# Optimization experiments

Hardware: AMD Instinct MI355X
Metric: run time of the kernel (lower is better)

The kernel has to match this reference:

```python
import jax, jax.numpy as jnp
import numpy as np

N, IN, HID, H, OUT = 5000, 64, 32, 4, 64
NEG_SLOPE = 0.2  # LeakyReLU slope used by GAT
MASK_VAL = -1e9


def setup_inputs() -> dict:
    key = jax.random.key(0)
    ks = jax.random.split(key, 8)
    adj = (jax.random.uniform(ks[0], (N, N)) < 0.02).astype(jnp.float32)
    adj = jnp.maximum(adj, jnp.eye(N, dtype=jnp.float32))
    h = jax.random.normal(ks[1], (N, IN), dtype=jnp.float32)
    # layer 1 params: W1 [IN, H*HID], attention vectors a1_* [H, HID]
    W1 = jax.random.normal(ks[2], (IN, H * HID), dtype=jnp.float32) / np.sqrt(IN)
    a1_src = jax.random.normal(ks[3], (H, HID), dtype=jnp.float32) / np.sqrt(HID)
    a1_dst = jax.random.normal(ks[4], (H, HID), dtype=jnp.float32) / np.sqrt(HID)
    # layer 2 params: single head, W2 [H*HID, OUT]
    W2 = jax.random.normal(ks[5], (H * HID, OUT), dtype=jnp.float32) / np.sqrt(H * HID)
    a2_src = jax.random.normal(ks[6], (1, OUT), dtype=jnp.float32) / np.sqrt(OUT)
    a2_dst = jax.random.normal(ks[7], (1, OUT), dtype=jnp.float32) / np.sqrt(OUT)
    return {"adj": adj, "h": h, "W1": W1, "a1_src": a1_src, "a1_dst": a1_dst,
            "W2": W2, "a2_src": a2_src, "a2_dst": a2_dst}


def gat_conv(adj, x, W, a_src, a_dst, heads, out_dim):
    n = x.shape[0]
    Wh = (x @ W).reshape(n, heads, out_dim)              # [N, H, F']
    s_src = jnp.einsum('nhf,hf->nh', Wh, a_src)          # score contribution of node as center i
    s_dst = jnp.einsum('nhf,hf->nh', Wh, a_dst)          # contribution of node as neighbor j
    e = s_src[:, None, :] + s_dst[None, :, :]            # [N, N, H]
    e = jax.nn.leaky_relu(e, NEG_SLOPE)
    e = jnp.where(adj[:, :, None] > 0, e, MASK_VAL)
    alpha = jax.nn.softmax(e, axis=1)                    # softmax over neighbors j
    out = jnp.einsum('ijh,jhf->ihf', alpha, Wh)          # aggregate
    return out.reshape(n, heads * out_dim)               # concat heads


def reference(adj, h, W1, a1_src, a1_dst, W2, a2_src, a2_dst):
    x = gat_conv(adj, h, W1, a1_src, a1_dst, H, HID)     # [N, H*HID]
    x = jax.nn.elu(x)
    out = gat_conv(adj, x, W2, a2_src, a2_dst, 1, OUT)   # [N, OUT]
    return out
```

## Files before the change

### kernel.cpp

```cpp
#include <hip/hip_runtime.h>
#include <math.h>

#define NN   5000
#define INF_ 64
#define HID  32
#define NH   4
#define OUTF 64
#define NEG  0.2f
#define CAP  256

typedef float nt4 __attribute__((ext_vector_type(4)));

__device__ inline float wred_sum(float v) {
#pragma unroll
    for (int off = 32; off > 0; off >>= 1) v += __shfl_down(v, off, 64);
    return v;
}

__device__ inline unsigned mask4(nt4 v) {
    return (v.x > 0.f ? 1u : 0u) | (v.y > 0.f ? 2u : 0u) |
           (v.z > 0.f ? 4u : 0u) | (v.w > 0.f ? 8u : 0u);
}

__global__ __launch_bounds__(256) void k1(const float* __restrict__ adj,
        const float* __restrict__ h, const float* __restrict__ W1,
        const float* __restrict__ a1s, const float* __restrict__ a1d,
        int* __restrict__ counts, int* __restrict__ idx,
        float* __restrict__ Wh1, float* __restrict__ s1s, float* __restrict__ s1d) {
    const int i = blockIdx.x, t = threadIdx.x;
    const int lane = t & 63, wave = t >> 6;
    __shared__ int nbs[CAP];
    __shared__ int wt4[4];
    const nt4* row4 = (const nt4*)(adj + (size_t)i * NN);
    nt4 v0 = __builtin_nontemporal_load(&row4[t]);
    nt4 v1 = __builtin_nontemporal_load(&row4[t + 256]);
    nt4 v2 = __builtin_nontemporal_load(&row4[t + 512]);
    nt4 v3 = __builtin_nontemporal_load(&row4[t + 768]);
    nt4 v4 = {0.f, 0.f, 0.f, 0.f};
    if (t < NN / 4 - 1024) v4 = __builtin_nontemporal_load(&row4[t + 1024]);
    const float hreg = h[(size_t)i * INF_ + lane];
    if (t < 128) {
        float acc = 0.f;
#pragma unroll
        for (int k = 0; k < INF_; ++k) acc += __shfl(hreg, k, 64) * W1[k * (NH * HID) + t];
        Wh1[(size_t)i * (NH * HID) + t] = acc;
        const int hd = t >> 5, f = t & 31;
        float vs = acc * a1s[hd * HID + f];
        float vd = acc * a1d[hd * HID + f];
#pragma unroll
        for (int off = 16; off > 0; off >>= 1) {
            vs += __shfl_down(vs, off, 32);
            vd += __shfl_down(vd, off, 32);
        }
        if (f == 0) { s1s[i * NH + hd] = vs; s1d[i * NH + hd] = vd; }
    }
    const unsigned m20 = mask4(v0) | (mask4(v1) << 4) | (mask4(v2) << 8) |
                         (mask4(v3) << 12) | (mask4(v4) << 16);
    const int cl = __popc(m20);
    int incl = cl;
#pragma unroll
    for (int off = 1; off < 64; off <<= 1) {
        int u = __shfl_up(incl, off, 64);
        if (lane >= off) incl += u;
    }
    if (lane == 63) wt4[wave] = incl;
    __syncthreads();
    int base = 0;
#pragma unroll
    for (int w = 0; w < 4; ++w) base += (w < wave) ? wt4[w] : 0;
    int p = base + (incl - cl);
    unsigned m = m20;
    while (m) {
        const int b = __ffs(m) - 1; m &= m - 1;
        const int nid = 4 * (t + (b >> 2) * 256) + (b & 3);
        if (p < CAP) nbs[p] = nid;
        ++p;
    }
    __syncthreads();
    const int tot = wt4[0] + wt4[1] + wt4[2] + wt4[3];
    const int c = tot < CAP ? tot : CAP;
    if (t == 0) counts[i] = c;
    int4* my4 = (int4*)(idx + (size_t)i * CAP);
    for (int e = t; e < ((c + 3) >> 2); e += 256) my4[e] = ((const int4*)nbs)[e];
}

__global__ __launch_bounds__(256) void k2(const int* __restrict__ counts,
        const int* __restrict__ idx, const float* __restrict__ Wh1,
        const float* __restrict__ s1s, const float* __restrict__ s1d,
        const float* __restrict__ W2, const float* __restrict__ a2s,
        const float* __restrict__ a2d, float* __restrict__ Wh2,
        float* __restrict__ s2s, float* __restrict__ s2d) {
    const int i = blockIdx.x, t = threadIdx.x;
    const int lane = t & 63, wave = t >> 6;
    const int c = counts[i];
    const int cp = (c + 3) & ~3;
    __shared__ int   nb[CAP];
    __shared__ float sc[NH][CAP + 1];
    __shared__ float aggf[4][128];
    __shared__ float xs[128];
    __shared__ float redh[4 * NH];
    __shared__ float pw[4][64];
    const float4 ss = ((const float4*)s1s)[i];
    const float4* s1d4 = (const float4*)s1d;
    const int* my = idx + (size_t)i * CAP;
    float l0 = 0.f, l1 = 0.f, l2 = 0.f, l3 = 0.f;
    for (int e = t; e < c; e += 256) {
        const int j = my[e];
        nb[e] = j;
        const float4 sd = s1d4[j];
        float w0 = ss.x + sd.x, w1 = ss.y + sd.y, w2 = ss.z + sd.z, w3 = ss.w + sd.w;
        w0 = (w0 >= 0.f) ? w0 : NEG * w0;
        w1 = (w1 >= 0.f) ? w1 : NEG * w1;
        w2 = (w2 >= 0.f) ? w2 : NEG * w2;
        w3 = (w3 >= 0.f) ? w3 : NEG * w3;
        const float p0 = __expf(w0), p1 = __expf(w1), p2 = __expf(w2), p3 = __expf(w3);
        sc[0][e] = p0; sc[1][e] = p1; sc[2][e] = p2; sc[3][e] = p3;
        l0 += p0; l1 += p1; l2 += p2; l3 += p3;
    }
    for (int e = c + t; e < cp; e += 256) {
        nb[e] = 0;
        sc[0][e] = 0.f; sc[1][e] = 0.f; sc[2][e] = 0.f; sc[3][e] = 0.f;
    }
    l0 = wred_sum(l0); l1 = wred_sum(l1); l2 = wred_sum(l2); l3 = wred_sum(l3);
    if (lane == 0) {
        redh[wave * NH + 0] = l0; redh[wave * NH + 1] = l1;
        redh[wave * NH + 2] = l2; redh[wave * NH + 3] = l3;
    }
    __syncthreads();
    {
        const float4* Wh1v = (const float4*)Wh1;
        const int half = lane >> 5, fi = lane & 31, hd = fi >> 3;
        const int g4 = cp >> 2;
        const int gw = (g4 + 3) >> 2;
        int g = wave * gw;
        const int gend = min(g4, wave * gw + gw);
        float4 a0 = {0.f,0.f,0.f,0.f}, a1 = a0, a2 = a0, a3 = a0;
        for (; g + 1 < gend; g += 2) {
            const int e = 4 * g;
            const int j0 = nb[e + half],     j1 = nb[e + 2 + half];
            const int j2 = nb[e + 4 + half], j3 = nb[e + 6 + half];
            const float p0 = sc[hd][e + half],     p1 = sc[hd][e + 2 + half];
            const float p2 = sc[hd][e + 4 + half], p3 = sc[hd][e + 6 + half];
            const float4 w0 = Wh1v[(size_t)j0 * 32 + fi];
            const float4 w1 = Wh1v[(size_t)j1 * 32 + fi];
            const float4 w2 = Wh1v[(size_t)j2 * 32 + fi];
            const float4 w3 = Wh1v[(size_t)j3 * 32 + fi];
            a0.x += p0 * w0.x; a0.y += p0 * w0.y; a0.z += p0 * w0.z; a0.w += p0 * w0.w;
            a1.x += p1 * w1.x; a1.y += p1 * w1.y; a1.z += p1 * w1.z; a1.w += p1 * w1.w;
            a2.x += p2 * w2.x; a2.y += p2 * w2.y; a2.z += p2 * w2.z; a2.w += p2 * w2.w;
            a3.x += p3 * w3.x; a3.y += p3 * w3.y; a3.z += p3 * w3.z; a3.w += p3 * w3.w;
        }
        if (g < gend) {
            const int e = 4 * g;
            const int j0 = nb[e + half], j1 = nb[e + 2 + half];
            const float p0 = sc[hd][e + half], p1 = sc[hd][e + 2 + half];
            const float4 w0 = Wh1v[(size_t)j0 * 32 + fi];
            const float4 w1 = Wh1v[(size_t)j1 * 32 + fi];
            a0.x += p0 * w0.x; a0.y += p0 * w0.y; a0.z += p0 * w0.z; a0.w += p0 * w0.w;
            a1.x += p1 * w1.x; a1.y += p1 * w1.y; a1.z += p1 * w1.z; a1.w += p1 * w1.w;
        }
        float4 aa;
        aa.x = (a0.x + a1.x) + (a2.x + a3.x);
        aa.y = (a0.y + a1.y) + (a2.y + a3.y);
        aa.z = (a0.z + a1.z) + (a2.z + a3.z);
        aa.w = (a0.w + a1.w) + (a2.w + a3.w);
        aa.x += __shfl_xor(aa.x, 32, 64);
        aa.y += __shfl_xor(aa.y, 32, 64);
        aa.z += __shfl_xor(aa.z, 32, 64);
        aa.w += __shfl_xor(aa.w, 32, 64);
        if (lane < 32) ((float4*)aggf[wave])[lane] = aa;
    }
    __syncthreads();
    if (t < 128) {
        const int hh = t >> 5;
        const float lh = redh[hh] + redh[NH + hh] + redh[2 * NH + hh] + redh[3 * NH + hh];
        float o = aggf[0][t] + aggf[1][t] + aggf[2][t] + aggf[3][t];
        o = o / lh;
        o = (o > 0.f) ? o : expm1f(o);
        xs[t] = o;
    }
    __syncthreads();
    {
        float pa = 0.f;
#pragma unroll
        for (int k = 0; k < 32; ++k)
            pa += xs[wave * 32 + k] * W2[(wave * 32 + k) * OUTF + lane];
        pw[wave][lane] = pa;
    }
    __syncthreads();
    if (t < 64) {
        float w = pw[0][t] + pw[1][t] + pw[2][t] + pw[3][t];
        Wh2[(size_t)i * OUTF + t] = w;
        float vs = wred_sum(w * a2s[t]);
        float vd = wred_sum(w * a2d[t]);
        if (t == 0) { s2s[i] = vs; s2d[i] = vd; }
    }
}

__global__ __launch_bounds__(128) void k3(const int* __restrict__ counts,
        const int* __restrict__ idx, const float* __restrict__ Wh2,
        const float* __restrict__ s2s, const float* __restrict__ s2d,
        float* __restrict__ out) {
    const int i = blockIdx.x, t = threadIdx.x;
    const int lane = t & 63, wave = t >> 6;
    const int c = counts[i];
    const int cp = (c + 3) & ~3;
    __shared__ int   nb[CAP];
    __shared__ float sc[CAP];
    __shared__ float red[2];
    __shared__ float agg[2][64];
    const float si = s2s[i];
    const int* my = idx + (size_t)i * CAP;
    float lsum = 0.f;
    for (int e = t; e < c; e += 128) {
        const int j = my[e];
        nb[e] = j;
        float v = si + s2d[j];
        v = (v >= 0.f) ? v : NEG * v;
        const float p = __expf(v);
        sc[e] = p;
        lsum += p;
    }
    for (int e = c + t; e < cp; e += 128) { nb[e] = 0; sc[e] = 0.f; }
    lsum = wred_sum(lsum);
    if (lane == 0) red[wave] = lsum;
    __syncthreads();
    const float4* Wh2v = (const float4*)Wh2;
    const int qi = lane >> 4, fi = lane & 15;
    const int g4 = cp >> 2;
    const int gw = (g4 + 1) >> 1;
    int g = wave * gw;
    const int gend = min(g4, wave * gw + gw);
    float4 a0 = {0.f,0.f,0.f,0.f}, a1 = a0;
    for (; g + 1 < gend; g += 2) {
        const int eA = 4 * g + qi, eB = 4 * g + 4 + qi;
        const int jA = nb[eA], jB = nb[eB];
        const float pA = sc[eA], pB = sc[eB];
        const float4 wA = Wh2v[(size_t)jA * 16 + fi];
        const float4 wB = Wh2v[(size_t)jB * 16 + fi];
        a0.x += pA * wA.x; a0.y += pA * wA.y; a0.z += pA * wA.z; a0.w += pA * wA.w;
        a1.x += pB * wB.x; a1.y += pB * wB.y; a1.z += pB * wB.z; a1.w += pB * wB.w;
    }
    if (g < gend) {
        const int eA = 4 * g + qi;
        const int jA = nb[eA];
        const float pA = sc[eA];
        const float4 wA = Wh2v[(size_t)jA * 16 + fi];
        a0.x += pA * wA.x; a0.y += pA * wA.y; a0.z += pA * wA.z; a0.w += pA * wA.w;
    }
    float4 aa;
    aa.x = a0.x + a1.x; aa.y = a0.y + a1.y; aa.z = a0.z + a1.z; aa.w = a0.w + a1.w;
#pragma unroll
    for (int off = 16; off <= 32; off <<= 1) {
        aa.x += __shfl_xor(aa.x, off, 64);
        aa.y += __shfl_xor(aa.y, off, 64);
        aa.z += __shfl_xor(aa.z, off, 64);
        aa.w += __shfl_xor(aa.w, off, 64);
    }
    if (lane < 16) ((float4*)agg[wave])[lane] = aa;
    __syncthreads();
    if (t < 64) {
        const float ls = red[0] + red[1];
        const float s = agg[0][t] + agg[1][t];
        out[(size_t)i * OUTF + t] = s / ls;
    }
}

extern "C" void kernel_launch(void* const* d_in, const int* in_sizes, int n_in,
                              void* d_out, int out_size, void* d_ws, size_t ws_size,
                              hipStream_t stream) {
    const float* adj = (const float*)d_in[0];
    const float* h   = (const float*)d_in[1];
    const float* W1  = (const float*)d_in[2];
    const float* a1s = (const float*)d_in[3];
    const float* a1d = (const float*)d_in[4];
    const float* W2  = (const float*)d_in[5];
    const float* a2s = (const float*)d_in[6];
    const float* a2d = (const float*)d_in[7];
    float* out = (float*)d_out;

    char* p = (char*)d_ws;
    float* Wh1 = (float*)p; p += (size_t)NN * 128 * 4;
    float* Wh2 = (float*)p; p += (size_t)NN * OUTF * 4;
    float* s1s = (float*)p; p += (size_t)NN * NH * 4;
    float* s1d = (float*)p; p += (size_t)NN * NH * 4;
    float* s2s = (float*)p; p += (size_t)NN * 4;
    float* s2d = (float*)p; p += (size_t)NN * 4;
    int*   cnt = (int*)p;   p += (size_t)NN * 4;
    int*   idx = (int*)p;   p += (size_t)NN * CAP * 4;

    k1<<<NN, 256, 0, stream>>>(adj, h, W1, a1s, a1d, cnt, idx, Wh1, s1s, s1d);
    k2<<<NN, 256, 0, stream>>>(cnt, idx, Wh1, s1s, s1d, W2, a2s, a2d, Wh2, s2s, s2d);
    k3<<<NN, 128, 0, stream>>>(cnt, idx, Wh2, s2s, s2d, out);
}
```

Before: 189.4 us.

## Fuse three GAT kernels into one persistent cooperative kernel with grid syncs

Replaces the three separate launches (adjacency compaction and layer-1 projection, layer-1 aggregation plus layer-2 projection, layer-2 aggregation) with one persistent cooperative kernel. Blocks loop over nodes in grid-stride fashion and phases are separated by grid-wide barriers. This removes launch overhead and the kernel-boundary drain between stages. The costs are grid-sync latency, per-node __syncthreads loops in a persistent grid, a union of shared memory across phases, and layer-2 aggregation now running with 256 threads instead of 128.

```diff
diff --git a/kernel.cpp b/kernel.cpp
--- a/kernel.cpp
+++ b/kernel.cpp
@@ -1,5 +1,8 @@
 #include <hip/hip_runtime.h>
+#include <hip/hip_cooperative_groups.h>
 #include <math.h>
+
+namespace cg = cooperative_groups;
 
 #define NN   5000
 #define INF_ 64
@@ -22,247 +25,245 @@
            (v.z > 0.f ? 4u : 0u) | (v.w > 0.f ? 8u : 0u);
 }
 
-__global__ __launch_bounds__(256) void k1(const float* __restrict__ adj,
-        const float* __restrict__ h, const float* __restrict__ W1,
-        const float* __restrict__ a1s, const float* __restrict__ a1d,
-        int* __restrict__ counts, int* __restrict__ idx,
-        float* __restrict__ Wh1, float* __restrict__ s1s, float* __restrict__ s1d) {
-    const int i = blockIdx.x, t = threadIdx.x;
-    const int lane = t & 63, wave = t >> 6;
-    __shared__ int nbs[CAP];
-    __shared__ int wt4[4];
-    const nt4* row4 = (const nt4*)(adj + (size_t)i * NN);
-    nt4 v0 = __builtin_nontemporal_load(&row4[t]);
-    nt4 v1 = __builtin_nontemporal_load(&row4[t + 256]);
-    nt4 v2 = __builtin_nontemporal_load(&row4[t + 512]);
-    nt4 v3 = __builtin_nontemporal_load(&row4[t + 768]);
-    nt4 v4 = {0.f, 0.f, 0.f, 0.f};
-    if (t < NN / 4 - 1024) v4 = __builtin_nontemporal_load(&row4[t + 1024]);
-    const float hreg = h[(size_t)i * INF_ + lane];
-    if (t < 128) {
-        float acc = 0.f;
-#pragma unroll
-        for (int k = 0; k < INF_; ++k) acc += __shfl(hreg, k, 64) * W1[k * (NH * HID) + t];
-        Wh1[(size_t)i * (NH * HID) + t] = acc;
-        const int hd = t >> 5, f = t & 31;
-        float vs = acc * a1s[hd * HID + f];
-        float vd = acc * a1d[hd * HID + f];
-#pragma unroll
-        for (int off = 16; off > 0; off >>= 1) {
-            vs += __shfl_down(vs, off, 32);
-            vd += __shfl_down(vd, off, 32);
-        }
-        if (f == 0) { s1s[i * NH + hd] = vs; s1d[i * NH + hd] = vd; }
+union alignas(16) SMem {
+    struct { int nbs[CAP]; int wt4[4]; } p1;
+    struct { int nb[CAP]; float sc[NH][CAP + 1]; float aggf[4][128];
+             float xs[128]; float redh[4 * NH]; float pw[4][64]; } p2;
+    struct { int nb[CAP]; float sc[CAP]; float red[4]; float agg[4][64]; } p3;
+};
+
+__global__ __launch_bounds__(256) void fused(
+        const float* __restrict__ adj, const float* __restrict__ h,
+        const float* __restrict__ W1, const float* __restrict__ a1s,
+        const float* __restrict__ a1d, const float* __restrict__ W2,
+        const float* __restrict__ a2s, const float* __restrict__ a2d,
+        float* __restrict__ out, float* __restrict__ Wh1, float* __restrict__ Wh2,
+        float* __restrict__ s1s, float* __restrict__ s1d,
+        float* __restrict__ s2s, float* __restrict__ s2d,
+        int* __restrict__ counts, int* __restrict__ idx) {
+    cg::grid_group gg = cg::this_grid();
+    const int t = threadIdx.x, lane = t & 63, wave = t >> 6;
+    __shared__ SMem sm;
+
+    for (int i = blockIdx.x; i < NN; i += gridDim.x) {
+        const nt4* row4 = (const nt4*)(adj + (size_t)i * NN);
+        nt4 v0 = __builtin_nontemporal_load(&row4[t]);
+        nt4 v1 = __builtin_nontemporal_load(&row4[t + 256]);
+        nt4 v2 = __builtin_nontemporal_load(&row4[t + 512]);
+        nt4 v3 = __builtin_nontemporal_load(&row4[t + 768]);
+        nt4 v4 = {0.f, 0.f, 0.f, 0.f};
+        if (t < NN / 4 - 1024) v4 = __builtin_nontemporal_load(&row4[t + 1024]);
+        const float hreg = h[(size_t)i * INF_ + lane];
+        if (t < 128) {
+            float acc = 0.f;
+#pragma unroll
+            for (int k = 0; k < INF_; ++k) acc += __shfl(hreg, k, 64) * W1[k * (NH * HID) + t];
+            Wh1[(size_t)i * (NH * HID) + t] = acc;
+            const int hd = t >> 5, f = t & 31;
+            float vs = acc * a1s[hd * HID + f];
+            float vd = acc * a1d[hd * HID + f];
+#pragma unroll
+            for (int off = 16; off > 0; off >>= 1) {
+                vs += __shfl_down(vs, off, 32);
+                vd += __shfl_down(vd, off, 32);
+            }
+            if (f == 0) { s1s[i * NH + hd] = vs; s1d[i * NH + hd] = vd; }
+        }
+        const unsigned m20 = mask4(v0) | (mask4(v1) << 4) | (mask4(v2) << 8) |
+                             (mask4(v3) << 12) | (mask4(v4) << 16);
+        const int cl = __popc(m20);
+        int incl = cl;
+#pragma unroll
+        for (int off = 1; off < 64; off <<= 1) {
+            int u = __shfl_up(incl, off, 64);
+            if (lane >= off) incl += u;
+        }
+        if (lane == 63) sm.p1.wt4[wave] = incl;
+        __syncthreads();
+        int base = 0;
+#pragma unroll
+        for (int w = 0; w < 4; ++w) base += (w < wave) ? sm.p1.wt4[w] : 0;
+        int p = base + (incl - cl);
+        unsigned m = m20;
+        while (m) {
+            const int b = __ffs(m) - 1; m &= m - 1;
+            const int nid = 4 * (t + (b >> 2) * 256) + (b & 3);
+            if (p < CAP) sm.p1.nbs[p] = nid;
+            ++p;
+        }
+        __syncthreads();
+        const int tot = sm.p1.wt4[0] + sm.p1.wt4[1] + sm.p1.wt4[2] + sm.p1.wt4[3];
+        const int c = tot < CAP ? tot : CAP;
+        if (t == 0) counts[i] = c;
+        int4* my4 = (int4*)(idx + (size_t)i * CAP);
+        for (int e = t; e < ((c + 3) >> 2); e += 256) my4[e] = ((const int4*)sm.p1.nbs)[e];
+        __syncthreads();
     }
-    const unsigned m20 = mask4(v0) | (mask4(v1) << 4) | (mask4(v2) << 8) |
-                         (mask4(v3) << 12) | (mask4(v4) << 16);
-    const int cl = __popc(m20);
-    int incl = cl;
-#pragma unroll
-    for (int off = 1; off < 64; off <<= 1) {
-        int u = __shfl_up(incl, off, 64);
-        if (lane >= off) incl += u;
+    __threadfence();
+    gg.sync();
+
+    for (int i = blockIdx.x; i < NN; i += gridDim.x) {
+        const int c = counts[i];
+        const int cp = (c + 3) & ~3;
+        const float4 ss = ((const float4*)s1s)[i];
+        const float4* s1d4 = (const float4*)s1d;
+        const int* my = idx + (size_t)i * CAP;
+        float l0 = 0.f, l1 = 0.f, l2 = 0.f, l3 = 0.f;
+        for (int e = t; e < c; e += 256) {
+            const int j = my[e];
+            sm.p2.nb[e] = j;
+            const float4 sd = s1d4[j];
+            float w0 = ss.x + sd.x, w1 = ss.y + sd.y, w2 = ss.z + sd.z, w3 = ss.w + sd.w;
+            w0 = (w0 >= 0.f) ? w0 : NEG * w0;
+            w1 = (w1 >= 0.f) ? w1 : NEG * w1;
+            w2 = (w2 >= 0.f) ? w2 : NEG * w2;
+            w3 = (w3 >= 0.f) ? w3 : NEG * w3;
+            const float p0 = __expf(w0), p1 = __expf(w1), p2 = __expf(w2), p3 = __expf(w3);
+            sm.p2.sc[0][e] = p0; sm.p2.sc[1][e] = p1; sm.p2.sc[2][e] = p2; sm.p2.sc[3][e] = p3;
+            l0 += p0; l1 += p1; l2 += p2; l3 += p3;
+        }
+        for (int e = c + t; e < cp; e += 256) {
+            sm.p2.nb[e] = 0;
+            sm.p2.sc[0][e] = 0.f; sm.p2.sc[1][e] = 0.f; sm.p2.sc[2][e] = 0.f; sm.p2.sc[3][e] = 0.f;
+        }
+        l0 = wred_sum(l0); l1 = wred_sum(l1); l2 = wred_sum(l2); l3 = wred_sum(l3);
+        if (lane == 0) {
+            sm.p2.redh[wave * NH + 0] = l0; sm.p2.redh[wave * NH + 1] = l1;
+            sm.p2.redh[wave * NH + 2] = l2; sm.p2.redh[wave * NH + 3] = l3;
+        }
+        __syncthreads();
+        {
+            const float4* Wh1v = (const float4*)Wh1;
+            const int half = lane >> 5, fi = lane & 31, hd = fi >> 3;
+            const int g4 = cp >> 2;
+            const int gw = (g4 + 3) >> 2;
+            int g = wave * gw;
+            const int gend = min(g4, wave * gw + gw);
+            float4 a0 = {0.f,0.f,0.f,0.f}, a1 = a0, a2 = a0, a3 = a0;
+            for (; g + 1 < gend; g += 2) {
+                const int e = 4 * g;
+                const int j0 = sm.p2.nb[e + half],     j1 = sm.p2.nb[e + 2 + half];
+                const int j2 = sm.p2.nb[e + 4 + half], j3 = sm.p2.nb[e + 6 + half];
+                const float p0 = sm.p2.sc[hd][e + half],     p1 = sm.p2.sc[hd][e + 2 + half];
+                const float p2 = sm.p2.sc[hd][e + 4 + half], p3 = sm.p2.sc[hd][e + 6 + half];
+                const float4 w0 = Wh1v[(size_t)j0 * 32 + fi];
+                const float4 w1 = Wh1v[(size_t)j1 * 32 + fi];
+                const float4 w2 = Wh1v[(size_t)j2 * 32 + fi];
+                const float4 w3 = Wh1v[(size_t)j3 * 32 + fi];
+                a0.x += p0 * w0.x; a0.y += p0 * w0.y; a0.z += p0 * w0.z; a0.w += p0 * w0.w;
+                a1.x += p1 * w1.x; a1.y += p1 * w1.y; a1.z += p1 * w1.z; a1.w += p1 * w1.w;
+                a2.x += p2 * w2.x; a2.y += p2 * w2.y; a2.z += p2 * w2.z; a2.w += p2 * w2.w;
+                a3.x += p3 * w3.x; a3.y += p3 * w3.y; a3.z += p3 * w3.z; a3.w += p3 * w3.w;
+            }
+            if (g < gend) {
+                const int e = 4 * g;
+                const int j0 = sm.p2.nb[e + half], j1 = sm.p2.nb[e + 2 + half];
+                const float p0 = sm.p2.sc[hd][e + half], p1 = sm.p2.sc[hd][e + 2 + half];
+                const float4 w0 = Wh1v[(size_t)j0 * 32 + fi];
+                const float4 w1 = Wh1v[(size_t)j1 * 32 + fi];
+                a0.x += p0 * w0.x; a0.y += p0 * w0.y; a0.z += p0 * w0.z; a0.w += p0 * w0.w;
+                a1.x += p1 * w1.x; a1.y += p1 * w1.y; a1.z += p1 * w1.z; a1.w += p1 * w1.w;
+            }
+            float4 aa;
+            aa.x = (a0.x + a1.x) + (a2.x + a3.x);
+            aa.y = (a0.y + a1.y) + (a2.y + a3.y);
+            aa.z = (a0.z + a1.z) + (a2.z + a3.z);
+            aa.w = (a0.w + a1.w) + (a2.w + a3.w);
+            aa.x += __shfl_xor(aa.x, 32, 64);
+            aa.y += __shfl_xor(aa.y, 32, 64);
+            aa.z += __shfl_xor(aa.z, 32, 64);
+            aa.w += __shfl_xor(aa.w, 32, 64);
+            if (lane < 32) ((float4*)sm.p2.aggf[wave])[lane] = aa;
+        }
+        __syncthreads();
+        if (t < 128) {
+            const int hh = t >> 5;
+            const float lh = sm.p2.redh[hh] + sm.p2.redh[NH + hh] +
+                             sm.p2.redh[2 * NH + hh] + sm.p2.redh[3 * NH + hh];
+            float o = sm.p2.aggf[0][t] + sm.p2.aggf[1][t] + sm.p2.aggf[2][t] + sm.p2.aggf[3][t];
+            o = o / lh;
+            o = (o > 0.f) ? o : expm1f(o);
+            sm.p2.xs[t] = o;
+        }
+        __syncthreads();
+        {
+            float pa = 0.f;
+#pragma unroll
+            for (int k = 0; k < 32; ++k)
+                pa += sm.p2.xs[wave * 32 + k] * W2[(wave * 32 + k) * OUTF + lane];
+            sm.p2.pw[wave][lane] = pa;
+        }
+        __syncthreads();
+        if (t < 64) {
+            float w = sm.p2.pw[0][t] + sm.p2.pw[1][t] + sm.p2.pw[2][t] + sm.p2.pw[3][t];
+            Wh2[(size_t)i * OUTF + t] = w;
+            float vs = wred_sum(w * a2s[t]);
+            float vd = wred_sum(w * a2d[t]);
+            if (t == 0) { s2s[i] = vs; s2d[i] = vd; }
+        }
     }
-    if (lane == 63) wt4[wave] = incl;
-    __syncthreads();
-    int base = 0;
-#pragma unroll
-    for (int w = 0; w < 4; ++w) base += (w < wave) ? wt4[w] : 0;
-    int p = base + (incl - cl);
-    unsigned m = m20;
-    while (m) {
-        const int b = __ffs(m) - 1; m &= m - 1;
-        const int nid = 4 * (t + (b >> 2) * 256) + (b & 3);
-        if (p < CAP) nbs[p] = nid;
-        ++p;
-    }
-    __syncthreads();
-    const int tot = wt4[0] + wt4[1] + wt4[2] + wt4[3];
-    const int c = tot < CAP ? tot : CAP;
-    if (t == 0) counts[i] = c;
-    int4* my4 = (int4*)(idx + (size_t)i * CAP);
-    for (int e = t; e < ((c + 3) >> 2); e += 256) my4[e] = ((const int4*)nbs)[e];
-}
-
-__global__ __launch_bounds__(256) void k2(const int* __restrict__ counts,
-        const int* __restrict__ idx, const float* __restrict__ Wh1,
-        const float* __restrict__ s1s, const float* __restrict__ s1d,
-        const float* __restrict__ W2, const float* __restrict__ a2s,
-        const float* __restrict__ a2d, float* __restrict__ Wh2,
-        float* __restrict__ s2s, float* __restrict__ s2d) {
-    const int i = blockIdx.x, t = threadIdx.x;
-    const int lane = t & 63, wave = t >> 6;
-    const int c = counts[i];
-    const int cp = (c + 3) & ~3;
-    __shared__ int   nb[CAP];
-    __shared__ float sc[NH][CAP + 1];
-    __shared__ float aggf[4][128];
-    __shared__ float xs[128];
-    __shared__ float redh[4 * NH];
-    __shared__ float pw[4][64];
-    const float4 ss = ((const float4*)s1s)[i];
-    const float4* s1d4 = (const float4*)s1d;
-    const int* my = idx + (size_t)i * CAP;
-    float l0 = 0.f, l1 = 0.f, l2 = 0.f, l3 = 0.f;
-    for (int e = t; e < c; e += 256) {
-        const int j = my[e];
-        nb[e] = j;
-        const float4 sd = s1d4[j];
-        float w0 = ss.x + sd.x, w1 = ss.y + sd.y, w2 = ss.z + sd.z, w3 = ss.w + sd.w;
-        w0 = (w0 >= 0.f) ? w0 : NEG * w0;
-        w1 = (w1 >= 0.f) ? w1 : NEG * w1;
-        w2 = (w2 >= 0.f) ? w2 : NEG * w2;
-        w3 = (w3 >= 0.f) ? w3 : NEG * w3;
-        const float p0 = __expf(w0), p1 = __expf(w1), p2 = __expf(w2), p3 = __expf(w3);
-        sc[0][e] = p0; sc[1][e] = p1; sc[2][e] = p2; sc[3][e] = p3;
-        l0 += p0; l1 += p1; l2 += p2; l3 += p3;
-    }
-    for (int e = c + t; e < cp; e += 256) {
-        nb[e] = 0;
-        sc[0][e] = 0.f; sc[1][e] = 0.f; sc[2][e] = 0.f; sc[3][e] = 0.f;
-    }
-    l0 = wred_sum(l0); l1 = wred_sum(l1); l2 = wred_sum(l2); l3 = wred_sum(l3);
-    if (lane == 0) {
-        redh[wave * NH + 0] = l0; redh[wave * NH + 1] = l1;
-        redh[wave * NH + 2] = l2; redh[wave * NH + 3] = l3;
-    }
-    __syncthreads();
-    {
-        const float4* Wh1v = (const float4*)Wh1;
-        const int half = lane >> 5, fi = lane & 31, hd = fi >> 3;
+    __threadfence();
+    gg.sync();
+
+    for (int i = blockIdx.x; i < NN; i += gridDim.x) {
+        const int c = counts[i];
+        const int cp = (c + 3) & ~3;
+        const float si = s2s[i];
+        const int* my = idx + (size_t)i * CAP;
+        float lsum = 0.f;
+        for (int e = t; e < c; e += 256) {
+            const int j = my[e];
+            sm.p3.nb[e] = j;
+            float v = si + s2d[j];
+            v = (v >= 0.f) ? v : NEG * v;
+            const float p = __expf(v);
+            sm.p3.sc[e] = p;
+            lsum += p;
+        }
+        for (int e = c + t; e < cp; e += 256) { sm.p3.nb[e] = 0; sm.p3.sc[e] = 0.f; }
+        lsum = wred_sum(lsum);
+        if (lane == 0) sm.p3.red[wave] = lsum;
+        __syncthreads();
+        const float4* Wh2v = (const float4*)Wh2;
+        const int qi = lane >> 4, fi = lane & 15;
         const int g4 = cp >> 2;
         const int gw = (g4 + 3) >> 2;
         int g = wave * gw;
         const int gend = min(g4, wave * gw + gw);
-        float4 a0 = {0.f,0.f,0.f,0.f}, a1 = a0, a2 = a0, a3 = a0;
+        float4 a0 = {0.f,0.f,0.f,0.f}, a1 = a0;
         for (; g + 1 < gend; g += 2) {
-            const int e = 4 * g;
-            const int j0 = nb[e + half],     j1 = nb[e + 2 + half];
-            const int j2 = nb[e + 4 + half], j3 = nb[e + 6 + half];
-            const float p0 = sc[hd][e + half],     p1 = sc[hd][e + 2 + half];
-            const float p2 = sc[hd][e + 4 + half], p3 = sc[hd][e + 6 + half];
-            const float4 w0 = Wh1v[(size_t)j0 * 32 + fi];
-            const float4 w1 = Wh1v[(size_t)j1 * 32 + fi];
-            const float4 w2 = Wh1v[(size_t)j2 * 32 + fi];
-            const float4 w3 = Wh1v[(size_t)j3 * 32 + fi];
-            a0.x += p0 * w0.x; a0.y += p0 * w0.y; a0.z += p0 * w0.z; a0.w += p0 * w0.w;
-            a1.x += p1 * w1.x; a1.y += p1 * w1.y; a1.z += p1 * w1.z; a1.w += p1 * w1.w;
-            a2.x += p2 * w2.x; a2.y += p2 * w2.y; a2.z += p2 * w2.z; a2.w += p2 * w2.w;
-            a3.x += p3 * w3.x; a3.y += p3 * w3.y; a3.z += p3 * w3.z; a3.w += p3 * w3.w;
+            const int eA = 4 * g + qi, eB = 4 * g + 4 + qi;
+            const int jA = sm.p3.nb[eA], jB = sm.p3.nb[eB];
+            const float pA = sm.p3.sc[eA], pB = sm.p3.sc[eB];
+            const float4 wA = Wh2v[(size_t)jA * 16 + fi];
+            const float4 wB = Wh2v[(size_t)jB * 16 + fi];
+            a0.x += pA * wA.x; a0.y += pA * wA.y; a0.z += pA * wA.z; a0.w += pA * wA.w;
+            a1.x += pB * wB.x; a1.y += pB * wB.y; a1.z += pB * wB.z; a1.w += pB * wB.w;
         }
         if (g < gend) {
-            const int e = 4 * g;
-            const int j0 = nb[e + half], j1 = nb[e + 2 + half];
-            const float p0 = sc[hd][e + half], p1 = sc[hd][e + 2 + half];
-            const float4 w0 = Wh1v[(size_t)j0 * 32 + fi];
-            const float4 w1 = Wh1v[(size_t)j1 * 32 + fi];
-            a0.x += p0 * w0.x; a0.y += p0 * w0.y; a0.z += p0 * w0.z; a0.w += p0 * w0.w;
-            a1.x += p1 * w1.x; a1.y += p1 * w1.y; a1.z += p1 * w1.z; a1.w += p1 * w1.w;
+            const int eA = 4 * g + qi;
+            const int jA = sm.p3.nb[eA];
+            const float pA = sm.p3.sc[eA];
+            const float4 wA = Wh2v[(size_t)jA * 16 + fi];
+            a0.x += pA * wA.x; a0.y += pA * wA.y; a0.z += pA * wA.z; a0.w += pA * wA.w;
         }
         float4 aa;
-        aa.x = (a0.x + a1.x) + (a2.x + a3.x);
-        aa.y = (a0.y + a1.y) + (a2.y + a3.y);
-        aa.z = (a0.z + a1.z) + (a2.z + a3.z);
-        aa.w = (a0.w + a1.w) + (a2.w + a3.w);
-        aa.x += __shfl_xor(aa.x, 32, 64);
-        aa.y += __shfl_xor(aa.y, 32, 64);
-        aa.z += __shfl_xor(aa.z, 32, 64);
-        aa.w += __shfl_xor(aa.w, 32, 64);
-        if (lane < 32) ((float4*)aggf[wave])[lane] = aa;
-    }
-    __syncthreads();
-    if (t < 128) {
-        const int hh = t >> 5;
-        const float lh = redh[hh] + redh[NH + hh] + redh[2 * NH + hh] + redh[3 * NH + hh];
-        float o = aggf[0][t] + aggf[1][t] + aggf[2][t] + aggf[3][t];
-        o = o / lh;
-        o = (o > 0.f) ? o : expm1f(o);
-        xs[t] = o;
-    }
-    __syncthreads();
-    {
-        float pa = 0.f;
-#pragma unroll
-        for (int k = 0; k < 32; ++k)
-            pa += xs[wave * 32 + k] * W2[(wave * 32 + k) * OUTF + lane];
-        pw[wave][lane] = pa;
-    }
-    __syncthreads();
-    if (t < 64) {
-        float w = pw[0][t] + pw[1][t] + pw[2][t] + pw[3][t];
-        Wh2[(size_t)i * OUTF + t] = w;
-        float vs = wred_sum(w * a2s[t]);
-        float vd = wred_sum(w * a2d[t]);
-        if (t == 0) { s2s[i] = vs; s2d[i] = vd; }
-    }
-}
-
-__global__ __launch_bounds__(128) void k3(const int* __restrict__ counts,
-        const int* __restrict__ idx, const float* __restrict__ Wh2,
-        const float* __restrict__ s2s, const float* __restrict__ s2d,
-        float* __restrict__ out) {
-    const int i = blockIdx.x, t = threadIdx.x;
-    const int lane = t & 63, wave = t >> 6;
-    const int c = counts[i];
-    const int cp = (c + 3) & ~3;
-    __shared__ int   nb[CAP];
-    __shared__ float sc[CAP];
-    __shared__ float red[2];
-    __shared__ float agg[2][64];
-    const float si = s2s[i];
-    const int* my = idx + (size_t)i * CAP;
-    float lsum = 0.f;
-    for (int e = t; e < c; e += 128) {
-        const int j = my[e];
-        nb[e] = j;
-        float v = si + s2d[j];
-        v = (v >= 0.f) ? v : NEG * v;
-        const float p = __expf(v);
-        sc[e] = p;
-        lsum += p;
-    }
-    for (int e = c + t; e < cp; e += 128) { nb[e] = 0; sc[e] = 0.f; }
-    lsum = wred_sum(lsum);
-    if (lane == 0) red[wave] = lsum;
-    __syncthreads();
-    const float4* Wh2v = (const float4*)Wh2;
-    const int qi = lane >> 4, fi = lane & 15;
-    const int g4 = cp >> 2;
-    const int gw = (g4 + 1) >> 1;
-    int g = wave * gw;
-    const int gend = min(g4, wave * gw + gw);
-    float4 a0 = {0.f,0.f,0.f,0.f}, a1 = a0;
-    for (; g + 1 < gend; g += 2) {
-        const int eA = 4 * g + qi, eB = 4 * g + 4 + qi;
-        const int jA = nb[eA], jB = nb[eB];
-        const float pA = sc[eA], pB = sc[eB];
-        const float4 wA = Wh2v[(size_t)jA * 16 + fi];
-        const float4 wB = Wh2v[(size_t)jB * 16 + fi];
-        a0.x += pA * wA.x; a0.y += pA * wA.y; a0.z += pA * wA.z; a0.w += pA * wA.w;
-        a1.x += pB * wB.x; a1.y += pB * wB.y; a1.z += pB * wB.z; a1.w += pB * wB.w;
-    }
-    if (g < gend) {
-        const int eA = 4 * g + qi;
-        const int jA = nb[eA];
-        const float pA = sc[eA];
-        const float4 wA = Wh2v[(size_t)jA * 16 + fi];
-        a0.x += pA * wA.x; a0.y += pA * wA.y; a0.z += pA * wA.z; a0.w += pA * wA.w;
-    }
-    float4 aa;
-    aa.x = a0.x + a1.x; aa.y = a0.y + a1.y; aa.z = a0.z + a1.z; aa.w = a0.w + a1.w;
-#pragma unroll
-    for (int off = 16; off <= 32; off <<= 1) {
-        aa.x += __shfl_xor(aa.x, off, 64);
-        aa.y += __shfl_xor(aa.y, off, 64);
-        aa.z += __shfl_xor(aa.z, off, 64);
-        aa.w += __shfl_xor(aa.w, off, 64);
-    }
-    if (lane < 16) ((float4*)agg[wave])[lane] = aa;
-    __syncthreads();
-    if (t < 64) {
-        const float ls = red[0] + red[1];
-        const float s = agg[0][t] + agg[1][t];
-        out[(size_t)i * OUTF + t] = s / ls;
+        aa.x = a0.x + a1.x; aa.y = a0.y + a1.y; aa.z = a0.z + a1.z; aa.w = a0.w + a1.w;
+#pragma unroll
+        for (int off = 16; off <= 32; off <<= 1) {
+            aa.x += __shfl_xor(aa.x, off, 64);
+            aa.y += __shfl_xor(aa.y, off, 64);
+            aa.z += __shfl_xor(aa.z, off, 64);
+            aa.w += __shfl_xor(aa.w, off, 64);
+        }
+        if (lane < 16) ((float4*)sm.p3.agg[wave])[lane] = aa;
+        __syncthreads();
+        if (t < 64) {
+            const float ls = sm.p3.red[0] + sm.p3.red[1] + sm.p3.red[2] + sm.p3.red[3];
+            const float s = sm.p3.agg[0][t] + sm.p3.agg[1][t] + sm.p3.agg[2][t] + sm.p3.agg[3][t];
+            out[(size_t)i * OUTF + t] = s / ls;
+        }
+        __syncthreads();
     }
 }
 
@@ -289,7 +290,25 @@
     int*   cnt = (int*)p;   p += (size_t)NN * 4;
     int*   idx = (int*)p;   p += (size_t)NN * CAP * 4;
 
-    k1<<<NN, 256, 0, stream>>>(adj, h, W1, a1s, a1d, cnt, idx, Wh1, s1s, s1d);
-    k2<<<NN, 256, 0, stream>>>(cnt, idx, Wh1, s1s, s1d, W2, a2s, a2d, Wh2, s2s, s2d);
-    k3<<<NN, 128, 0, stream>>>(cnt, idx, Wh2, s2s, s2d, out);
+    static int grid = 0;
+    if (grid == 0) {
+        int dev = 0;
+        hipGetDevice(&dev);
+        hipDeviceProp_t prop;
+        hipGetDeviceProperties(&prop, dev);
+        int nb = 0;
+        hipOccupancyMaxActiveBlocksPerMultiprocessor(&nb, fused, 256, 0);
+        if (nb < 1) nb = 1;
+        long g = (long)nb * prop.multiProcessorCount;
+        if (g > NN) g = NN;
+        grid = (int)g;
+    }
+
+    void* args[] = {
+        (void*)&adj, (void*)&h, (void*)&W1, (void*)&a1s, (void*)&a1d,
+        (void*)&W2, (void*)&a2s, (void*)&a2d, (void*)&out,
+        (void*)&Wh1, (void*)&Wh2, (void*)&s1s, (void*)&s1d,
+        (void*)&s2s, (void*)&s2d, (void*)&cnt, (void*)&idx
+    };
+    hipLaunchCooperativeKernel(fused, dim3(grid), dim3(256), args, 0, stream);
 }
```

Result: slower. 507.8 us (+168.1%).
